# Kernel tuning notes

Measured on AMD Instinct MI355X. Metric: run time of the kernel, lower is better.

The kernel has to match this reference:

```python
import jax, jax.numpy as jnp
import numpy as np

B, H, W, C = 16, 56, 56, 512
HEADS, WIN = 16, 7
HID = 2048
EPS = 1e-5


def _rel_pos_index(win):
    coords = np.stack(np.meshgrid(np.arange(win), np.arange(win), indexing='ij'))  # 2,w,w
    cf = coords.reshape(2, -1)  # 2, w*w
    rel = (cf[:, :, None] - cf[:, None, :]).transpose(1, 2, 0).astype(np.int64)  # N,N,2
    rel[..., 0] += win - 1
    rel[..., 1] += win - 1
    rel[..., 0] *= 2 * win - 1
    return jnp.asarray(rel.sum(-1))  # N,N


def setup_inputs() -> dict:
    key = jax.random.key(0)
    ks = jax.random.split(key, 12)
    s = 0.02
    return {
        'x': jax.random.normal(ks[0], (B, H * W, C), jnp.float32),
        'norm1_w': jnp.ones((C,), jnp.float32),
        'norm1_b': jnp.zeros((C,), jnp.float32),
        'qkv_w': jax.random.normal(ks[1], (3 * C, C), jnp.float32) * s,
        'qkv_b': jnp.zeros((3 * C,), jnp.float32),
        'proj_w': jax.random.normal(ks[2], (C, C), jnp.float32) * s,
        'proj_b': jnp.zeros((C,), jnp.float32),
        'rel_bias_table': jax.random.normal(ks[3], ((2 * WIN - 1) ** 2, HEADS), jnp.float32) * s,
        'norm2_w': jnp.ones((C,), jnp.float32),
        'norm2_b': jnp.zeros((C,), jnp.float32),
        'fc1_w': jax.random.normal(ks[4], (HID, C), jnp.float32) * s,
        'fc1_b': jnp.zeros((HID,), jnp.float32),
        'fc2_w': jax.random.normal(ks[5], (C, HID), jnp.float32) * s,
        'fc2_b': jnp.zeros((C,), jnp.float32),
        'rel_pos_index': _rel_pos_index(WIN),
    }


def _ln(x, w, b):
    m = jnp.mean(x, -1, keepdims=True)
    v = jnp.mean((x - m) ** 2, -1, keepdims=True)
    return (x - m) * jax.lax.rsqrt(v + EPS) * w + b


def reference(x, norm1_w, norm1_b, qkv_w, qkv_b, proj_w, proj_b, rel_bias_table,
              norm2_w, norm2_b, fc1_w, fc1_b, fc2_w, fc2_b, rel_pos_index):
    N = WIN * WIN
    hd = C // HEADS
    shortcut = x
    h = _ln(x, norm1_w, norm1_b).reshape(B, H, W, C)
    # window partition -> (nW*B, N, C)
    h = h.reshape(B, H // WIN, WIN, W // WIN, WIN, C).transpose(0, 1, 3, 2, 4, 5)
    xw = h.reshape(-1, N, C)
    Bw = xw.shape[0]
    qkv = (xw @ qkv_w.T + qkv_b).reshape(Bw, N, 3, HEADS, hd).transpose(2, 0, 3, 1, 4)
    q, k, v = qkv[0], qkv[1], qkv[2]  # (Bw, heads, N, hd)
    q = q * (hd ** -0.5)
    attn = jnp.einsum('bhnd,bhmd->bhnm', q, k)
    bias = rel_bias_table[rel_pos_index.reshape(-1)].reshape(N, N, HEADS).transpose(2, 0, 1)
    attn = jax.nn.softmax(attn + bias[None], axis=-1)
    out = jnp.einsum('bhnm,bhmd->bhnd', attn, v).transpose(0, 2, 1, 3).reshape(Bw, N, C)
    out = out @ proj_w.T + proj_b
    # window reverse -> (B, H*W, C)
    out = out.reshape(B, H // WIN, W // WIN, WIN, WIN, C).transpose(0, 1, 3, 2, 4, 5)
    out = out.reshape(B, H * W, C)
    x = shortcut + out
    h2 = _ln(x, norm2_w, norm2_b)
    h2 = jax.nn.gelu(h2 @ fc1_w.T + fc1_b, approximate=False) @ fc2_w.T + fc2_b
    return x + h2
```

## Files before the change

### kernel.cpp

```cpp
#include <hip/hip_runtime.h>
#include <stdint.h>

#define B_    16
#define C_    512
#define HEADS 16
#define NTOK  49
#define ROWS  (16*56*56)

typedef __attribute__((ext_vector_type(8))) __bf16 bf16x8;
typedef __attribute__((ext_vector_type(4))) float  f32x4;
typedef __attribute__((ext_vector_type(8))) unsigned short u16x8;
typedef __attribute__((ext_vector_type(4))) unsigned short u16x4;

__device__ __forceinline__ unsigned short f2bf(float f) {
  union { float f; uint32_t u; } x; x.f = f;
  uint32_t r = x.u + 0x7FFFu + ((x.u >> 16) & 1u);
  return (unsigned short)(r >> 16);
}
__device__ __forceinline__ float bf2f(unsigned short u) {
  union { uint32_t u; float f; } x; x.u = ((uint32_t)u) << 16;
  return x.f;
}

template<int EPI>
__global__ __launch_bounds__(512, 2)
void gemm_bt(const unsigned short* __restrict__ A,
             const unsigned short* __restrict__ Bt,
             const float* __restrict__ bias,
             const float* __restrict__ res,
             void* __restrict__ outp,
             int N, int K, int ldb, int nbn)
{
  __shared__ __align__(16) unsigned short As[2][256*64];
  __shared__ __align__(16) unsigned short Bs[2][256*64];

  const int nwg = gridDim.x;
  const int q8 = nwg >> 3, r8 = nwg & 7;
  const int xcd = blockIdx.x & 7, ixc = blockIdx.x >> 3;
  const int l = (xcd < r8 ? xcd * (q8 + 1) : r8 * (q8 + 1) + (xcd - r8) * q8) + ixc;
  const int bm = l / nbn, bn = l % nbn;

  const int tid  = threadIdx.x;
  const int wave = tid >> 6;
  const int lane = tid & 63;
  const int wr = wave >> 2, wc = wave & 3;

  const unsigned short* Ag = A  + (size_t)bm * 256 * K;
  const unsigned short* Bg = Bt + (size_t)bn * 256 * ldb;

  f32x4 acc[8][4] = {};
  const int fr = lane & 15;
  const int kq = lane >> 4;
  const int sx = fr & 7;

  auto STAGE = [&](int buf, int t) {
    const int k0 = t << 6;
    #pragma unroll
    for (int li = 0; li < 4; ++li) {
      const int slot = tid + li * 512;
      const int r = slot >> 3;
      const int g = (slot & 7) ^ (r & 7);
      __builtin_amdgcn_global_load_lds(
        (const __attribute__((address_space(1))) void*)(Ag + (size_t)r * K + k0 + g * 8),
        (__attribute__((address_space(3))) void*)(&As[buf][(li * 512 + wave * 64) * 8]), 16, 0, 0);
    }
    #pragma unroll
    for (int li = 0; li < 4; ++li) {
      const int slot = tid + li * 512;
      const int r = slot >> 3;
      const int g = (slot & 7) ^ (r & 7);
      __builtin_amdgcn_global_load_lds(
        (const __attribute__((address_space(1))) void*)(Bg + (size_t)r * ldb + k0 + g * 8),
        (__attribute__((address_space(3))) void*)(&Bs[buf][(li * 512 + wave * 64) * 8]), 16, 0, 0);
    }
  };

  const int nt = K >> 6;
  STAGE(0, 0);
  for (int t = 0; t < nt; ++t) {
    const int c = t & 1;
    if (t + 1 < nt) {
      STAGE(c ^ 1, t + 1);
      asm volatile("s_waitcnt vmcnt(8)" ::: "memory");
    } else {
      asm volatile("s_waitcnt vmcnt(0)" ::: "memory");
    }
    __builtin_amdgcn_s_barrier();

    #pragma unroll
    for (int ks = 0; ks < 2; ++ks) {
      bf16x8 a[8], b[4];
      #pragma unroll
      for (int m = 0; m < 8; ++m)
        a[m] = *(const bf16x8*)&As[c][(wr * 128 + m * 16 + fr) * 64
                                      + (((ks * 4 + kq) ^ sx) * 8)];
      #pragma unroll
      for (int n = 0; n < 4; ++n)
        b[n] = *(const bf16x8*)&Bs[c][(wc * 64 + n * 16 + fr) * 64
                                      + (((ks * 4 + kq) ^ sx) * 8)];
      __builtin_amdgcn_s_setprio(1);
      #pragma unroll
      for (int m = 0; m < 8; ++m)
        #pragma unroll
        for (int n = 0; n < 4; ++n)
          acc[m][n] = __builtin_amdgcn_mfma_f32_16x16x32_bf16(a[m], b[n], acc[m][n], 0, 0, 0);
      __builtin_amdgcn_s_setprio(0);
    }

    asm volatile("s_waitcnt lgkmcnt(0)" ::: "memory");
    __builtin_amdgcn_s_barrier();
  }

  const int rq = lane >> 4;
  #pragma unroll
  for (int m = 0; m < 8; ++m) {
    #pragma unroll
    for (int n = 0; n < 4; ++n) {
      const int gcol = bn * 256 + wc * 64 + n * 16 + fr;
      const float bv = (EPI == 3) ? 0.f : bias[gcol];
      #pragma unroll
      for (int r = 0; r < 4; ++r) {
        const int grow = bm * 256 + wr * 128 + m * 16 + rq * 4 + r;
        const size_t off = (size_t)grow * N + gcol;
        float v = acc[m][n][r] + bv;
        if (EPI == 0) {
          ((unsigned short*)outp)[off] = f2bf(v);
        } else if (EPI == 1) {
          v = 0.5f * v * (1.0f + erff(v * 0.70710678118654752f));
          ((unsigned short*)outp)[off] = f2bf(v);
        } else {
          ((float*)outp)[off] = v + res[off];
        }
      }
    }
  }
}

__global__ __launch_bounds__(256)
void ln_bf16(const float* __restrict__ x, const float* __restrict__ w,
             const float* __restrict__ b, unsigned short* __restrict__ out)
{
  const int row  = blockIdx.x * 4 + (threadIdx.x >> 6);
  const int lane = threadIdx.x & 63;
  const float4* xr = (const float4*)(x + (size_t)row * C_);
  const float4 u = xr[lane * 2];
  const float4 v = xr[lane * 2 + 1];
  const float vals[8] = {u.x,u.y,u.z,u.w,v.x,v.y,v.z,v.w};
  float s = 0.f, s2 = 0.f;
  #pragma unroll
  for (int j = 0; j < 8; ++j) { s += vals[j]; s2 += vals[j]*vals[j]; }
  #pragma unroll
  for (int off = 1; off < 64; off <<= 1) {
    s  += __shfl_xor(s,  off);
    s2 += __shfl_xor(s2, off);
  }
  const float mean = s * (1.0f/512.0f);
  const float rstd = rsqrtf(s2 * (1.0f/512.0f) - mean*mean + 1e-5f);
  u16x8 o;
  #pragma unroll
  for (int j = 0; j < 8; ++j) {
    const int col = lane * 8 + j;
    o[j] = f2bf((vals[j] - mean) * rstd * w[col] + b[col]);
  }
  *(u16x8*)&out[(size_t)row * C_ + lane * 8] = o;
}

__global__ __launch_bounds__(512)
void attn_win2(const unsigned short* __restrict__ qkv,
               const unsigned short* __restrict__ biasBf,
               unsigned short* __restrict__ outb, int i0)
{
  __shared__ float  Ksh[8][NTOK*32];
  __shared__ float  Vsh[8][NTOK*32];
  __shared__ unsigned short Bsh[8][NTOK*NTOK];
  const int bi   = blockIdx.x;
  const int half = bi & 1, winl = bi >> 1;
  const int bbl = winl >> 6, wy = (winl >> 3) & 7, wx = winl & 7;
  const int wave = threadIdx.x >> 6, lane = threadIdx.x & 63;
  const int head = half * 8 + wave;

  for (int i = lane; i < NTOK*NTOK; i += 64)
    Bsh[wave][i] = biasBf[head * (NTOK*NTOK) + i];

  float q[32];
  size_t gl = 0, gg = 0;
  if (lane < NTOK) {
    const int r = lane / 7, c = lane % 7;
    gl = (size_t)bbl * 3136 + (size_t)((wy*7 + r) * 56 + (wx*7 + c));
    gg = gl + (size_t)i0 * 3136;
    const unsigned short* qp = qkv + gl * 1536 + head * 32;
    #pragma unroll
    for (int d = 0; d < 32; d += 4) {
      const u16x4 qv = *(const u16x4*)&qp[d];
      const u16x4 kv = *(const u16x4*)&qp[512 + d];
      const u16x4 vv = *(const u16x4*)&qp[1024 + d];
      #pragma unroll
      for (int e = 0; e < 4; ++e) {
        q[d+e] = bf2f(qv[e]);
        Ksh[wave][lane*32 + d + e] = bf2f(kv[e]);
        Vsh[wave][lane*32 + d + e] = bf2f(vv[e]);
      }
    }
  }
  if (lane < NTOK) {
    float s[NTOK];
    float mx = -1e30f;
    for (int j = 0; j < NTOK; ++j) {
      float dot = 0.f;
      #pragma unroll
      for (int d = 0; d < 32; ++d) dot += q[d] * Ksh[wave][j*32 + d];
      const float val = dot * 0.17677669529663687f
                      + bf2f(Bsh[wave][lane*NTOK + j]);
      s[j] = val;
      mx = fmaxf(mx, val);
    }
    float sum = 0.f;
    for (int j = 0; j < NTOK; ++j) { s[j] = __expf(s[j] - mx); sum += s[j]; }
    const float inv = 1.0f / sum;
    float o[32];
    #pragma unroll
    for (int d = 0; d < 32; ++d) o[d] = 0.f;
    for (int j = 0; j < NTOK; ++j) {
      const float p = s[j] * inv;
      #pragma unroll
      for (int d = 0; d < 32; ++d) o[d] += p * Vsh[wave][j*32 + d];
    }
    unsigned short* op = outb + gg * 512 + head * 32;
    #pragma unroll
    for (int d = 0; d < 32; d += 4) {
      u16x4 ov;
      #pragma unroll
      for (int e = 0; e < 4; ++e) ov[e] = f2bf(o[d+e]);
      *(u16x4*)&op[d] = ov;
    }
  }
}

__global__ void build_bias(const float* __restrict__ table, const int* __restrict__ idx,
                           unsigned short* __restrict__ biasBf)
{
  const int i = blockIdx.x * 256 + threadIdx.x;
  if (i >= HEADS * NTOK * NTOK) return;
  const int h  = i / (NTOK*NTOK);
  const int ij = i - h * (NTOK*NTOK);
  biasBf[i] = f2bf(table[idx[ij] * HEADS + h]);
}

__global__ void conv_bf16(const float* __restrict__ in, unsigned short* __restrict__ out, int n4)
{
  const int i = blockIdx.x * 256 + threadIdx.x;
  if (i >= n4) return;
  const float4 v = ((const float4*)in)[i];
  u16x4 o; o[0]=f2bf(v.x); o[1]=f2bf(v.y); o[2]=f2bf(v.z); o[3]=f2bf(v.w);
  ((u16x4*)out)[i] = o;
}

extern "C" void kernel_launch(void* const* d_in, const int* in_sizes, int n_in,
                              void* d_out, int out_size, void* d_ws, size_t ws_size,
                              hipStream_t stream)
{
  const float* x     = (const float*)d_in[0];
  const float* n1w   = (const float*)d_in[1];
  const float* n1b   = (const float*)d_in[2];
  const float* qkvw  = (const float*)d_in[3];
  const float* qkvb  = (const float*)d_in[4];
  const float* projw = (const float*)d_in[5];
  const float* projb = (const float*)d_in[6];
  const float* rbt   = (const float*)d_in[7];
  const float* n2w   = (const float*)d_in[8];
  const float* n2b   = (const float*)d_in[9];
  const float* fc1w  = (const float*)d_in[10];
  const float* fc1b  = (const float*)d_in[11];
  const float* fc2w  = (const float*)d_in[12];
  const float* fc2b  = (const float*)d_in[13];
  const int*   rpi   = (const int*)d_in[14];
  float* out = (float*)d_out;

  char* p = (char*)d_ws;
  auto alloc = [&](size_t bytes) -> char* {
    char* q = p; p += (bytes + 255) & ~(size_t)255; return q;
  };
  unsigned short* wqB  = (unsigned short*)alloc((size_t)1536 * 512 * 2);
  unsigned short* wpB  = (unsigned short*)alloc((size_t)512  * 512 * 2);
  unsigned short* w1B  = (unsigned short*)alloc((size_t)2048 * 512 * 2);
  unsigned short* w2B  = (unsigned short*)alloc((size_t)512  * 2048 * 2);
  unsigned short* biasBf = (unsigned short*)alloc((size_t)HEADS * NTOK * NTOK * 2);
  unsigned short* bufX = (unsigned short*)alloc((size_t)ROWS * 512 * 2);
  const size_t used = (size_t)(p - (char*)d_ws);
  const size_t Rbytes = (ws_size > used) ? ws_size - used : 0;
  unsigned short* R = (unsigned short*)p;

  int ic = 0;
  for (int c = 16; c >= 4; c >>= 1)
    if ((size_t)c * 3136 * 1536 * 2 <= Rbytes) { ic = c; break; }
  int hc = 0;
  for (int c = 2048; c >= 256; c >>= 1)
    if ((size_t)ROWS * c * 2 <= Rbytes) { hc = c; break; }
  if (ic == 0 || hc == 0) return;

  conv_bf16<<<(1536*512/4 + 255)/256, 256, 0, stream>>>(qkvw, wqB, 1536*512/4);
  conv_bf16<<<(512*512/4  + 255)/256, 256, 0, stream>>>(projw, wpB, 512*512/4);
  conv_bf16<<<(2048*512/4 + 255)/256, 256, 0, stream>>>(fc1w, w1B, 2048*512/4);
  conv_bf16<<<(512*2048/4 + 255)/256, 256, 0, stream>>>(fc2w, w2B, 512*2048/4);
  build_bias<<<(HEADS*NTOK*NTOK + 255)/256, 256, 0, stream>>>(rbt, rpi, biasBf);

  ln_bf16<<<ROWS/4, 256, 0, stream>>>(x, n1w, n1b, bufX);

  for (int i0 = 0; i0 < B_; i0 += ic) {
    const int nbm = ic * 3136 / 256, nbn = 6;
    gemm_bt<0><<<nbm * nbn, 512, 0, stream>>>(
        bufX + (size_t)i0*3136*512, wqB, qkvb, nullptr, R, 1536, 512, 512, nbn);
    attn_win2<<<ic*64*2, 512, 0, stream>>>(R, biasBf, bufX, i0);
  }

  gemm_bt<2><<<(ROWS/256) * 2, 512, 0, stream>>>(
      bufX, wpB, projb, x, out, 512, 512, 512, 2);

  ln_bf16<<<ROWS/4, 256, 0, stream>>>(out, n2w, n2b, bufX);

  for (int h0 = 0; h0 < 2048; h0 += hc) {
    gemm_bt<1><<<(ROWS/256) * (hc/256), 512, 0, stream>>>(
        bufX, w1B + (size_t)h0*512, fc1b + h0, nullptr, R, hc, 512, 512, hc/256);
    if (h0 == 0)
      gemm_bt<2><<<(ROWS/256) * 2, 512, 0, stream>>>(
          R, w2B + h0, fc2b, out, out, 512, hc, 2048, 2);
    else
      gemm_bt<3><<<(ROWS/256) * 2, 512, 0, stream>>>(
          R, w2B + h0, nullptr, out, out, 512, hc, 2048, 2);
  }
}
```

Before: 861.4 us.

## Shrink GEMM tiles to 128x128, gather windows in proj GEMM, simplify attention softmax

```diff
diff --git a/kernel.cpp b/kernel.cpp
--- a/kernel.cpp
+++ b/kernel.cpp
@@ -12,6 +12,9 @@
 typedef __attribute__((ext_vector_type(8))) unsigned short u16x8;
 typedef __attribute__((ext_vector_type(4))) unsigned short u16x4;
 
+#define AS1 __attribute__((address_space(1)))
+#define AS3 __attribute__((address_space(3)))
+
 __device__ __forceinline__ unsigned short f2bf(float f) {
   union { float f; uint32_t u; } x; x.f = f;
   uint32_t r = x.u + 0x7FFFu + ((x.u >> 16) & 1u);
@@ -22,8 +25,17 @@
   return x.f;
 }
 
-template<int EPI>
-__global__ __launch_bounds__(512, 2)
+__device__ __forceinline__ int winmap(int grow) {
+  const int b = grow / 3136;
+  const int pos = grow - b * 3136;
+  const int y = pos / 56, x = pos - y * 56;
+  const int win = (y / 7) * 8 + (x / 7);
+  const int r = (y % 7) * 7 + (x % 7);
+  return b * 3136 + win * 49 + r;
+}
+
+template<int EPI, int GATHER>
+__global__ __launch_bounds__(512, 4)
 void gemm_bt(const unsigned short* __restrict__ A,
              const unsigned short* __restrict__ Bt,
              const float* __restrict__ bias,
@@ -31,8 +43,8 @@
              void* __restrict__ outp,
              int N, int K, int ldb, int nbn)
 {
-  __shared__ __align__(16) unsigned short As[2][256*64];
-  __shared__ __align__(16) unsigned short Bs[2][256*64];
+  __shared__ __align__(16) unsigned short As[2][128*64];
+  __shared__ __align__(16) unsigned short Bs[2][128*64];
 
   const int nwg = gridDim.x;
   const int q8 = nwg >> 3, r8 = nwg & 7;
@@ -45,10 +57,20 @@
   const int lane = tid & 63;
   const int wr = wave >> 2, wc = wave & 3;
 
-  const unsigned short* Ag = A  + (size_t)bm * 256 * K;
-  const unsigned short* Bg = Bt + (size_t)bn * 256 * ldb;
-
-  f32x4 acc[8][4] = {};
+  const unsigned short* aSrc[2];
+  const unsigned short* bSrc[2];
+  #pragma unroll
+  for (int i = 0; i < 2; ++i) {
+    const int u = tid + i * 512;
+    const int rt = u >> 3;
+    const int g  = (u & 7) ^ (rt & 7);
+    int ga = bm * 128 + rt;
+    if (GATHER) ga = winmap(ga);
+    aSrc[i] = A  + (size_t)ga * K + g * 8;
+    bSrc[i] = Bt + (size_t)(bn * 128 + rt) * ldb + g * 8;
+  }
+
+  f32x4 acc[4][2] = {};
   const int fr = lane & 15;
   const int kq = lane >> 4;
   const int sx = fr & 7;
@@ -56,23 +78,15 @@
   auto STAGE = [&](int buf, int t) {
     const int k0 = t << 6;
     #pragma unroll
-    for (int li = 0; li < 4; ++li) {
-      const int slot = tid + li * 512;
-      const int r = slot >> 3;
-      const int g = (slot & 7) ^ (r & 7);
+    for (int i = 0; i < 2; ++i)
       __builtin_amdgcn_global_load_lds(
-        (const __attribute__((address_space(1))) void*)(Ag + (size_t)r * K + k0 + g * 8),
-        (__attribute__((address_space(3))) void*)(&As[buf][(li * 512 + wave * 64) * 8]), 16, 0, 0);
-    }
-    #pragma unroll
-    for (int li = 0; li < 4; ++li) {
-      const int slot = tid + li * 512;
-      const int r = slot >> 3;
-      const int g = (slot & 7) ^ (r & 7);
+        (const AS1 void*)(aSrc[i] + k0),
+        (AS3 void*)(&As[buf][(i * 512 + wave * 64) * 8]), 16, 0, 0);
+    #pragma unroll
+    for (int i = 0; i < 2; ++i)
       __builtin_amdgcn_global_load_lds(
-        (const __attribute__((address_space(1))) void*)(Bg + (size_t)r * ldb + k0 + g * 8),
-        (__attribute__((address_space(3))) void*)(&Bs[buf][(li * 512 + wave * 64) * 8]), 16, 0, 0);
-    }
+        (const AS1 void*)(bSrc[i] + k0),
+        (AS3 void*)(&Bs[buf][(i * 512 + wave * 64) * 8]), 16, 0, 0);
   };
 
   const int nt = K >> 6;
@@ -81,52 +95,55 @@
     const int c = t & 1;
     if (t + 1 < nt) {
       STAGE(c ^ 1, t + 1);
-      asm volatile("s_waitcnt vmcnt(8)" ::: "memory");
+      asm volatile("s_waitcnt vmcnt(4)" ::: "memory");
     } else {
       asm volatile("s_waitcnt vmcnt(0)" ::: "memory");
     }
     __builtin_amdgcn_s_barrier();
+    asm volatile("" ::: "memory");
 
     #pragma unroll
     for (int ks = 0; ks < 2; ++ks) {
-      bf16x8 a[8], b[4];
-      #pragma unroll
-      for (int m = 0; m < 8; ++m)
-        a[m] = *(const bf16x8*)&As[c][(wr * 128 + m * 16 + fr) * 64
+      bf16x8 a[4], b[2];
+      #pragma unroll
+      for (int m = 0; m < 4; ++m)
+        a[m] = *(const bf16x8*)&As[c][(wr * 64 + m * 16 + fr) * 64
                                       + (((ks * 4 + kq) ^ sx) * 8)];
       #pragma unroll
-      for (int n = 0; n < 4; ++n)
-        b[n] = *(const bf16x8*)&Bs[c][(wc * 64 + n * 16 + fr) * 64
+      for (int n = 0; n < 2; ++n)
+        b[n] = *(const bf16x8*)&Bs[c][(wc * 32 + n * 16 + fr) * 64
                                       + (((ks * 4 + kq) ^ sx) * 8)];
       __builtin_amdgcn_s_setprio(1);
       #pragma unroll
-      for (int m = 0; m < 8; ++m)
+      for (int m = 0; m < 4; ++m)
         #pragma unroll
-        for (int n = 0; n < 4; ++n)
+        for (int n = 0; n < 2; ++n)
           acc[m][n] = __builtin_amdgcn_mfma_f32_16x16x32_bf16(a[m], b[n], acc[m][n], 0, 0, 0);
       __builtin_amdgcn_s_setprio(0);
     }
 
     asm volatile("s_waitcnt lgkmcnt(0)" ::: "memory");
     __builtin_amdgcn_s_barrier();
+    asm volatile("" ::: "memory");
   }
 
   const int rq = lane >> 4;
   #pragma unroll
-  for (int m = 0; m < 8; ++m) {
-    #pragma unroll
-    for (int n = 0; n < 4; ++n) {
-      const int gcol = bn * 256 + wc * 64 + n * 16 + fr;
+  for (int m = 0; m < 4; ++m) {
+    #pragma unroll
+    for (int n = 0; n < 2; ++n) {
+      const int gcol = bn * 128 + wc * 32 + n * 16 + fr;
       const float bv = (EPI == 3) ? 0.f : bias[gcol];
       #pragma unroll
       for (int r = 0; r < 4; ++r) {
-        const int grow = bm * 256 + wr * 128 + m * 16 + rq * 4 + r;
+        const int grow = bm * 128 + wr * 64 + m * 16 + rq * 4 + r;
         const size_t off = (size_t)grow * N + gcol;
         float v = acc[m][n][r] + bv;
         if (EPI == 0) {
           ((unsigned short*)outp)[off] = f2bf(v);
         } else if (EPI == 1) {
-          v = 0.5f * v * (1.0f + erff(v * 0.70710678118654752f));
+          const float u2 = 1.5957691216f * v * (1.0f + 0.044715f * v * v);
+          v = v / (1.0f + __expf(-u2));
           ((unsigned short*)outp)[off] = f2bf(v);
         } else {
           ((float*)outp)[off] = v + res[off];
@@ -165,29 +182,27 @@
   *(u16x8*)&out[(size_t)row * C_ + lane * 8] = o;
 }
 
-__global__ __launch_bounds__(512)
-void attn_win2(const unsigned short* __restrict__ qkv,
+__global__ __launch_bounds__(256)
+void attn_win3(const unsigned short* __restrict__ qkv,
                const unsigned short* __restrict__ biasBf,
-               unsigned short* __restrict__ outb, int i0)
-{
-  __shared__ float  Ksh[8][NTOK*32];
-  __shared__ float  Vsh[8][NTOK*32];
-  __shared__ unsigned short Bsh[8][NTOK*NTOK];
-  const int bi   = blockIdx.x;
-  const int half = bi & 1, winl = bi >> 1;
+               unsigned short* __restrict__ woutb, int i0)
+{
+  __shared__ float Ksh[4][NTOK*32];
+  __shared__ float Vsh[4][NTOK*32];
+  __shared__ unsigned short Bsh[4][NTOK*NTOK];
+  const int bi = blockIdx.x;
+  const int qtr = bi & 3, winl = bi >> 2;
   const int bbl = winl >> 6, wy = (winl >> 3) & 7, wx = winl & 7;
   const int wave = threadIdx.x >> 6, lane = threadIdx.x & 63;
-  const int head = half * 8 + wave;
+  const int head = qtr * 4 + wave;
 
   for (int i = lane; i < NTOK*NTOK; i += 64)
     Bsh[wave][i] = biasBf[head * (NTOK*NTOK) + i];
 
   float q[32];
-  size_t gl = 0, gg = 0;
   if (lane < NTOK) {
     const int r = lane / 7, c = lane % 7;
-    gl = (size_t)bbl * 3136 + (size_t)((wy*7 + r) * 56 + (wx*7 + c));
-    gg = gl + (size_t)i0 * 3136;
+    const size_t gl = (size_t)bbl * 3136 + (size_t)((wy*7 + r) * 56 + (wx*7 + c));
     const unsigned short* qp = qkv + gl * 1536 + head * 32;
     #pragma unroll
     for (int d = 0; d < 32; d += 4) {
@@ -203,34 +218,29 @@
     }
   }
   if (lane < NTOK) {
-    float s[NTOK];
-    float mx = -1e30f;
+    float lsum = 0.f;
+    float o[32];
+    #pragma unroll
+    for (int d = 0; d < 32; ++d) o[d] = 0.f;
     for (int j = 0; j < NTOK; ++j) {
       float dot = 0.f;
       #pragma unroll
       for (int d = 0; d < 32; ++d) dot += q[d] * Ksh[wave][j*32 + d];
       const float val = dot * 0.17677669529663687f
                       + bf2f(Bsh[wave][lane*NTOK + j]);
-      s[j] = val;
-      mx = fmaxf(mx, val);
-    }
-    float sum = 0.f;
-    for (int j = 0; j < NTOK; ++j) { s[j] = __expf(s[j] - mx); sum += s[j]; }
-    const float inv = 1.0f / sum;
-    float o[32];
-    #pragma unroll
-    for (int d = 0; d < 32; ++d) o[d] = 0.f;
-    for (int j = 0; j < NTOK; ++j) {
-      const float p = s[j] * inv;
-      #pragma unroll
-      for (int d = 0; d < 32; ++d) o[d] += p * Vsh[wave][j*32 + d];
-    }
-    unsigned short* op = outb + gg * 512 + head * 32;
+      const float e = __expf(val);
+      lsum += e;
+      #pragma unroll
+      for (int d = 0; d < 32; ++d) o[d] += e * Vsh[wave][j*32 + d];
+    }
+    const float inv = 1.0f / lsum;
+    unsigned short* op = woutb
+        + ((size_t)((bbl + i0) * 64 + wy * 8 + wx) * 49 + lane) * 512 + head * 32;
     #pragma unroll
     for (int d = 0; d < 32; d += 4) {
       u16x4 ov;
       #pragma unroll
-      for (int e = 0; e < 4; ++e) ov[e] = f2bf(o[d+e]);
+      for (int e = 0; e < 4; ++e) ov[e] = f2bf(o[d+e] * inv);
       *(u16x4*)&op[d] = ov;
     }
   }
@@ -291,10 +301,10 @@
   unsigned short* R = (unsigned short*)p;
 
   int ic = 0;
-  for (int c = 16; c >= 4; c >>= 1)
+  for (int c = 16; c >= 2; c >>= 1)
     if ((size_t)c * 3136 * 1536 * 2 <= Rbytes) { ic = c; break; }
   int hc = 0;
-  for (int c = 2048; c >= 256; c >>= 1)
+  for (int c = 2048; c >= 128; c >>= 1)
     if ((size_t)ROWS * c * 2 <= Rbytes) { hc = c; break; }
   if (ic == 0 || hc == 0) return;
 
@@ -307,25 +317,25 @@
   ln_bf16<<<ROWS/4, 256, 0, stream>>>(x, n1w, n1b, bufX);
 
   for (int i0 = 0; i0 < B_; i0 += ic) {
-    const int nbm = ic * 3136 / 256, nbn = 6;
-    gemm_bt<0><<<nbm * nbn, 512, 0, stream>>>(
+    const int nbm = ic * 3136 / 128, nbn = 12;
+    gemm_bt<0,0><<<nbm * nbn, 512, 0, stream>>>(
         bufX + (size_t)i0*3136*512, wqB, qkvb, nullptr, R, 1536, 512, 512, nbn);
-    attn_win2<<<ic*64*2, 512, 0, stream>>>(R, biasBf, bufX, i0);
-  }
-
-  gemm_bt<2><<<(ROWS/256) * 2, 512, 0, stream>>>(
-      bufX, wpB, projb, x, out, 512, 512, 512, 2);
+    attn_win3<<<ic*64*4, 256, 0, stream>>>(R, biasBf, bufX, i0);
+  }
+
+  gemm_bt<2,1><<<(ROWS/128) * 4, 512, 0, stream>>>(
+      bufX, wpB, projb, x, out, 512, 512, 512, 4);
 
   ln_bf16<<<ROWS/4, 256, 0, stream>>>(out, n2w, n2b, bufX);
 
   for (int h0 = 0; h0 < 2048; h0 += hc) {
-    gemm_bt<1><<<(ROWS/256) * (hc/256), 512, 0, stream>>>(
-        bufX, w1B + (size_t)h0*512, fc1b + h0, nullptr, R, hc, 512, 512, hc/256);
+    gemm_bt<1,0><<<(ROWS/128) * (hc/128), 512, 0, stream>>>(
+        bufX, w1B + (size_t)h0*512, fc1b + h0, nullptr, R, hc, 512, 512, hc/128);
     if (h0 == 0)
-      gemm_bt<2><<<(ROWS/256) * 2, 512, 0, stream>>>(
-          R, w2B + h0, fc2b, out, out, 512, hc, 2048, 2);
+      gemm_bt<2,0><<<(ROWS/128) * 4, 512, 0, stream>>>(
+          R, w2B + h0, fc2b, out, out, 512, hc, 2048, 4);
     else
-      gemm_bt<3><<<(ROWS/256) * 2, 512, 0, stream>>>(
-          R, w2B + h0, nullptr, out, out, 512, hc, 2048, 2);
-  }
-}
+      gemm_bt<3,0><<<(ROWS/128) * 4, 512, 0, stream>>>(
+          R, w2B + h0, nullptr, out, out, 512, hc, 2048, 4);
+  }
+}
```

New measurement: 742.8 us. 1.16x faster.
